# Performance work log

Measured on AMD Instinct MI355X. Metric: run time of the kernel, lower is better.

Reference implementation:

```python
import jax, jax.numpy as jnp
import numpy as np

N_NODES = 100_000
N_EDGES = 3_200_000
EPS_BN = 1e-5
EPS_NORM = 1e-12


def _sage_conv(x, src, dst, ew, pw, pb, lw, lb, rw, n_nodes):
    # project=True: relu(Linear_in->in) applied to source features
    xp = jax.nn.relu(x @ pw + pb)                       # [N, in]
    msg = xp[src] * ew[:, None]                         # [E, in] gather + weight
    agg = jax.ops.segment_sum(msg, dst, num_segments=n_nodes)      # scatter-sum
    cnt = jax.ops.segment_sum(jnp.ones_like(ew), dst, num_segments=n_nodes)
    mean = agg / jnp.maximum(cnt, 1.0)[:, None]         # scatter-mean
    out = mean @ lw + lb + x @ rw                       # neighbor lin + root lin
    # normalize=True: L2 normalize rows
    nrm = jnp.sqrt(jnp.sum(out * out, axis=-1, keepdims=True))
    return out / jnp.maximum(nrm, EPS_NORM)


def setup_inputs() -> dict:
    key = jax.random.key(0)
    ks = jax.random.split(key, 20)
    d = {}
    d["h"] = jax.random.normal(ks[0], (N_NODES, 5), dtype=jnp.float32)
    d["edge_index"] = jax.random.randint(ks[1], (2, N_EDGES), 0, N_NODES, dtype=jnp.int32)
    d["edge_weight"] = jax.random.uniform(ks[2], (N_EDGES,), dtype=jnp.float32)
    # BatchNorm1d(5) params (conv2_norm in the source is unused in forward)
    d["bn_gamma"] = jnp.ones((5,), jnp.float32)
    d["bn_beta"] = jnp.zeros((5,), jnp.float32)

    def lin(k, fan_in, fan_out):
        return jax.random.normal(k, (fan_in, fan_out), jnp.float32) * (1.0 / np.sqrt(fan_in))

    # conv1: 5 -> 64 ; conv2: 64 -> 64 (fixing source bug) ; conv3: 64 -> 5
    dims = [(5, 64), (64, 64), (64, 5)]
    ki = 3
    for i, (fi, fo) in enumerate(dims, start=1):
        d[f"c{i}_pw"] = lin(ks[ki], fi, fi); ki += 1
        d[f"c{i}_pb"] = jnp.zeros((fi,), jnp.float32)
        d[f"c{i}_lw"] = lin(ks[ki], fi, fo); ki += 1
        d[f"c{i}_lb"] = jnp.zeros((fo,), jnp.float32)
        d[f"c{i}_rw"] = lin(ks[ki], fi, fo); ki += 1
    return d


def reference(h, edge_index, edge_weight, bn_gamma, bn_beta,
              c1_pw, c1_pb, c1_lw, c1_lb, c1_rw,
              c2_pw, c2_pb, c2_lw, c2_lb, c2_rw,
              c3_pw, c3_pb, c3_lw, c3_lb, c3_rw):
    src, dst = edge_index[0], edge_index[1]
    # BatchNorm1d (training-mode batch statistics, biased variance)
    mu = jnp.mean(h, axis=0)
    var = jnp.mean((h - mu) ** 2, axis=0)
    x = (h - mu) * jax.lax.rsqrt(var + EPS_BN) * bn_gamma + bn_beta

    x = jax.nn.relu(_sage_conv(x, src, dst, edge_weight, c1_pw, c1_pb, c1_lw, c1_lb, c1_rw, N_NODES))
    x = jax.nn.relu(_sage_conv(x, src, dst, edge_weight, c2_pw, c2_pb, c2_lw, c2_lb, c2_rw, N_NODES))
    x = _sage_conv(x, src, dst, edge_weight, c3_pw, c3_pb, c3_lw, c3_lb, c3_rw, N_NODES)
    # dropout omitted (deterministic / eval-mode reference)
    return x
```

## Files before the change

### kernel.cpp

```cpp
#include <hip/hip_runtime.h>
#include <hip/hip_bf16.h>

#define N_NODES 100000
#define N_EDGES 3200000
#define BSH 8
#define NB 391

typedef __hip_bfloat16 bf16;

#define RL(v, k) __int_as_float(__builtin_amdgcn_readlane(__float_as_int(v), (k)))

__device__ __forceinline__ float loadF(const void* p, long long i, int isf32) {
    if (isf32) return ((const float*)p)[i];
    unsigned short v = ((const unsigned short*)p)[i];
    union { unsigned u; float f; } c;
    c.u = ((unsigned)v) << 16;
    return c.f;
}

__device__ __forceinline__ unsigned packEdge(int s, float w) {
    bf16 b = __float2bfloat16(w);
    unsigned short bits = *(unsigned short*)&b;
    return ((unsigned)s << 15) | (unsigned)(bits & 0x7FFF);
}
__device__ __forceinline__ int edgeSrc(unsigned u) { return (int)(u >> 15); }
__device__ __forceinline__ float edgeW(unsigned u) {
    union { unsigned x; float f; } c;
    c.x = (u & 0x7FFFu) << 16;
    return c.f;
}

#define W_GAMMA 0
#define W_BETA 8
#define W_C1PW 16
#define W_C1PB 48
#define W_C1LW 56
#define W_C1LB 376
#define W_C1RW 440
#define W_C2PW 760
#define W_C2PB 4856
#define W_C2LW 4920
#define W_C2LB 9016
#define W_C2RW 9080
#define W_C3PW 13176
#define W_C3PB 17272
#define W_C3LW 17336
#define W_C3LB 17656
#define W_C3RW 17664

__global__ void detect_dtype(const void* ew, int* flag) {
    const unsigned short* u = (const unsigned short*)ew;
    int lane = threadIdx.x;
    int big = 0;
    for (int i = lane; i < 1024; i += 64) {
        unsigned short v = u[2 * i];
        int ex = (v >> 7) & 0xFF;
        if (ex >= 128) big++;
    }
#pragma unroll
    for (int o = 32; o; o >>= 1) big += __shfl_xor(big, o, 64);
    if (lane == 0) *flag = (big > 100) ? 1 : 0;
}

__global__ void cvt_weights(const int* flag,
                            const void* p0, const void* p1, const void* p2, const void* p3,
                            const void* p4, const void* p5, const void* p6, const void* p7,
                            const void* p8, const void* p9, const void* p10, const void* p11,
                            const void* p12, const void* p13, const void* p14, const void* p15,
                            const void* p16, float* __restrict__ wts) {
    const void* ptrs[17] = {p0, p1, p2, p3, p4, p5, p6, p7, p8,
                            p9, p10, p11, p12, p13, p14, p15, p16};
    const int sz[17] = {5, 5, 25, 5, 320, 64, 320, 4096, 64,
                        4096, 64, 4096, 4096, 64, 320, 5, 320};
    const int off[17] = {W_GAMMA, W_BETA, W_C1PW, W_C1PB, W_C1LW, W_C1LB, W_C1RW,
                         W_C2PW, W_C2PB, W_C2LW, W_C2LB, W_C2RW,
                         W_C3PW, W_C3PB, W_C3LW, W_C3LB, W_C3RW};
    int t = blockIdx.x;
    int isf32 = *flag;
    for (int i = threadIdx.x; i < sz[t]; i += blockDim.x)
        wts[off[t] + i] = loadF(ptrs[t], i, isf32);
}

__global__ void bn_stats(const void* __restrict__ h, const int* __restrict__ flag,
                         float* __restrict__ stats) {
    int isf32 = *flag;
    float s[5] = {0, 0, 0, 0, 0}, q[5] = {0, 0, 0, 0, 0};
    int tid = blockIdx.x * blockDim.x + threadIdx.x;
    int stride = gridDim.x * blockDim.x;
    for (int i = tid; i < N_NODES; i += stride) {
#pragma unroll
        for (int f = 0; f < 5; f++) {
            float v = loadF(h, i * 5 + f, isf32);
            s[f] += v;
            q[f] += v * v;
        }
    }
#pragma unroll
    for (int f = 0; f < 5; f++) {
#pragma unroll
        for (int o = 32; o; o >>= 1) {
            s[f] += __shfl_xor(s[f], o, 64);
            q[f] += __shfl_xor(q[f], o, 64);
        }
    }
    __shared__ float ls[4][10];
    int wave = threadIdx.x >> 6, lane = threadIdx.x & 63;
    if (lane == 0) {
#pragma unroll
        for (int f = 0; f < 5; f++) { ls[wave][f] = s[f]; ls[wave][5 + f] = q[f]; }
    }
    __syncthreads();
    if (threadIdx.x < 10) {
        float v = ls[0][threadIdx.x] + ls[1][threadIdx.x] + ls[2][threadIdx.x] + ls[3][threadIdx.x];
        int idx = (threadIdx.x < 5) ? threadIdx.x : (threadIdx.x - 5 + 8);
        atomicAdd(&stats[idx], v);
    }
}

__global__ void bn_proj1(const void* __restrict__ h, const int* __restrict__ flag,
                         const float* __restrict__ stats, const float* __restrict__ wts,
                         float* __restrict__ xbn, float* __restrict__ xp1) {
    __shared__ float s_sc[5], s_sb[5];
    if (threadIdx.x < 5) {
        int f = threadIdx.x;
        float mean = stats[f] / (float)N_NODES;
        float var = stats[8 + f] / (float)N_NODES - mean * mean;
        float sc = wts[W_GAMMA + f] * rsqrtf(var + 1e-5f);
        s_sc[f] = sc;
        s_sb[f] = wts[W_BETA + f] - mean * sc;
    }
    __syncthreads();
    int isf32 = *flag;
    int i = blockIdx.x * blockDim.x + threadIdx.x;
    if (i >= N_NODES) return;
    float x[5];
#pragma unroll
    for (int f = 0; f < 5; f++)
        x[f] = loadF(h, i * 5 + f, isf32) * s_sc[f] + s_sb[f];
#pragma unroll
    for (int f = 0; f < 5; f++) xbn[i * 5 + f] = x[f];
#pragma unroll
    for (int j = 0; j < 5; j++) {
        float a = wts[W_C1PB + j];
#pragma unroll
        for (int k = 0; k < 5; k++) a += x[k] * wts[W_C1PW + k * 5 + j];
        xp1[i * 8 + j] = fmaxf(a, 0.f);
    }
}

__global__ void __launch_bounds__(256) bucket_hist(const int* __restrict__ dst,
                                                   int* __restrict__ bucketCnt) {
    __shared__ int hcnt[NB];
    for (int i = threadIdx.x; i < NB; i += 256) hcnt[i] = 0;
    __syncthreads();
    int per = (N_EDGES + gridDim.x - 1) / gridDim.x;
    int s = blockIdx.x * per;
    int e = min(s + per, N_EDGES);
    for (int i = s + threadIdx.x; i < e; i += 256)
        atomicAdd(&hcnt[dst[i] >> BSH], 1);
    __syncthreads();
    for (int i = threadIdx.x; i < NB; i += 256)
        if (hcnt[i]) atomicAdd(&bucketCnt[i], hcnt[i]);
}

__global__ void __launch_bounds__(512) bucket_scan(const int* __restrict__ bucketCnt,
                                                   int* __restrict__ bucketStart,
                                                   int* __restrict__ bucketCursor) {
    int tid = threadIdx.x, lane = tid & 63, w = tid >> 6;
    int v = (tid < NB) ? bucketCnt[tid] : 0;
    int sc = v;
#pragma unroll
    for (int o = 1; o < 64; o <<= 1) {
        int t = __shfl_up(sc, o, 64);
        if (lane >= o) sc += t;
    }
    __shared__ int ws[8];
    if (lane == 63) ws[w] = sc;
    __syncthreads();
    if (w == 0) {
        int wv = (lane < 8) ? ws[lane] : 0;
        int s2 = wv;
#pragma unroll
        for (int o = 1; o < 8; o <<= 1) {
            int t = __shfl_up(s2, o, 64);
            if (lane >= o) s2 += t;
        }
        if (lane < 8) ws[lane] = s2;
    }
    __syncthreads();
    int woff = w ? ws[w - 1] : 0;
    int ex = woff + sc - v;
    if (tid < NB) {
        bucketStart[tid] = ex;
        bucketCursor[tid] = ex;
    }
    if (tid == 0) bucketStart[NB] = N_EDGES;
}

__global__ void __launch_bounds__(256) bucket_stage(const int* __restrict__ src,
                                                    const int* __restrict__ dst,
                                                    const void* __restrict__ ew,
                                                    const int* __restrict__ flag,
                                                    int* __restrict__ bucketCursor,
                                                    uint2* __restrict__ stage) {
    __shared__ int hcnt[NB], cur[NB];
    int isf32 = *flag;
    for (int i = threadIdx.x; i < NB; i += 256) hcnt[i] = 0;
    __syncthreads();
    int per = (N_EDGES + gridDim.x - 1) / gridDim.x;
    int s = blockIdx.x * per;
    int e = min(s + per, N_EDGES);
    for (int i = s + threadIdx.x; i < e; i += 256)
        atomicAdd(&hcnt[dst[i] >> BSH], 1);
    __syncthreads();
    for (int i = threadIdx.x; i < NB; i += 256)
        cur[i] = hcnt[i] ? atomicAdd(&bucketCursor[i], hcnt[i]) : 0;
    __syncthreads();
    for (int i = s + threadIdx.x; i < e; i += 256) {
        int d = dst[i];
        int slot = atomicAdd(&cur[d >> BSH], 1);
        stage[slot] = make_uint2((unsigned)d, packEdge(src[i], loadF(ew, i, isf32)));
    }
}

__global__ void __launch_bounds__(256) bucket_place(const uint2* __restrict__ stage,
                                                    const int* __restrict__ bucketStart,
                                                    int* __restrict__ start,
                                                    unsigned* __restrict__ perm) {
    int b = blockIdx.x, tid = threadIdx.x;
    int base = bucketStart[b];
    int cnt = bucketStart[b + 1] - base;
    int n0 = b << BSH;
    int nn = min(256, N_NODES - n0);
    __shared__ int lcnt[256], loff[256], ws[4];
    lcnt[tid] = 0;
    __syncthreads();
    for (int i = tid; i < cnt; i += 256)
        atomicAdd(&lcnt[stage[base + i].x & 255], 1);
    __syncthreads();
    int lane = tid & 63, w = tid >> 6;
    int v = lcnt[tid];
    int sc = v;
#pragma unroll
    for (int o = 1; o < 64; o <<= 1) {
        int t = __shfl_up(sc, o, 64);
        if (lane >= o) sc += t;
    }
    if (lane == 63) ws[w] = sc;
    __syncthreads();
    int woff = 0;
    for (int k = 0; k < w; k++) woff += ws[k];
    loff[tid] = woff + sc - v;
    __syncthreads();
    if (tid < nn) start[n0 + tid] = base + loff[tid];
    if (b == 0 && tid == 0) start[N_NODES] = N_EDGES;
    lcnt[tid] = 0;
    __syncthreads();
    for (int i = tid; i < cnt; i += 256) {
        uint2 sv = stage[base + i];
        int l = sv.x & 255;
        int p = atomicAdd(&lcnt[l], 1);
        perm[base + loff[l] + p] = sv.y;
    }
}

__global__ void __launch_bounds__(256) conv1_fused(const float* __restrict__ xp1,
                                                   const float* __restrict__ xbn,
                                                   const int* __restrict__ start,
                                                   const unsigned* __restrict__ perm,
                                                   const float* __restrict__ wts,
                                                   float* __restrict__ x1,
                                                   bf16* __restrict__ y2) {
    int lane = threadIdx.x & 63;
    int wid = __builtin_amdgcn_readfirstlane((blockIdx.x * blockDim.x + threadIdx.x) >> 6);
    int nw = (gridDim.x * blockDim.x) >> 6;
    float Wlw[5], Wrw[5];
#pragma unroll
    for (int k = 0; k < 5; k++) {
        Wlw[k] = wts[W_C1LW + k * 64 + lane];
        Wrw[k] = wts[W_C1RW + k * 64 + lane];
    }
    float lb = wts[W_C1LB + lane];
    float W1[64], W2[64];
#pragma unroll
    for (int k = 0; k < 64; k++) W1[k] = wts[W_C2PW + k * 64 + lane];
#pragma unroll
    for (int k = 0; k < 64; k++) W2[k] = wts[W_C2LW + k * 64 + lane];
    float pb = wts[W_C2PB + lane];
    for (int node = wid; node < N_NODES; node += nw) {
        int e0 = start[node], e1 = start[node + 1];
        float s0 = 0, s1 = 0, s2 = 0, s3 = 0, s4 = 0;
        for (int eb = e0; eb < e1; eb += 64) {
            int e = eb + lane;
            if (e < e1) {
                unsigned p = perm[e];
                float w = edgeW(p);
                const float* row = xp1 + (size_t)edgeSrc(p) * 8;
                float4 v4 = *(const float4*)row;
                float v5 = row[4];
                s0 += v4.x * w; s1 += v4.y * w; s2 += v4.z * w;
                s3 += v4.w * w; s4 += v5 * w;
            }
        }
#pragma unroll
        for (int o = 32; o; o >>= 1) {
            s0 += __shfl_xor(s0, o, 64);
            s1 += __shfl_xor(s1, o, 64);
            s2 += __shfl_xor(s2, o, 64);
            s3 += __shfl_xor(s3, o, 64);
            s4 += __shfl_xor(s4, o, 64);
        }
        float ic = 1.f / fmaxf((float)(e1 - e0), 1.f);
        float xb = (lane < 5) ? xbn[node * 5 + lane] : 0.f;
        float out = lb + s0 * ic * Wlw[0] + s1 * ic * Wlw[1] + s2 * ic * Wlw[2] +
                    s3 * ic * Wlw[3] + s4 * ic * Wlw[4];
#pragma unroll
        for (int k = 0; k < 5; k++) out += RL(xb, k) * Wrw[k];
        float ss = out * out;
#pragma unroll
        for (int o = 32; o; o >>= 1) ss += __shfl_xor(ss, o, 64);
        float xv = fmaxf(out / fmaxf(sqrtf(ss), 1e-12f), 0.f);
        x1[(size_t)node * 64 + lane] = xv;
        float a0 = pb, a1 = 0.f, a2 = 0.f, a3 = 0.f;
#pragma unroll
        for (int k = 0; k < 64; k += 4) {
            a0 += RL(xv, k) * W1[k];
            a1 += RL(xv, k + 1) * W1[k + 1];
            a2 += RL(xv, k + 2) * W1[k + 2];
            a3 += RL(xv, k + 3) * W1[k + 3];
        }
        float xp = fmaxf((a0 + a1) + (a2 + a3), 0.f);
        float b0 = 0.f, b1 = 0.f, b2 = 0.f, b3 = 0.f;
#pragma unroll
        for (int k = 0; k < 64; k += 4) {
            b0 += RL(xp, k) * W2[k];
            b1 += RL(xp, k + 1) * W2[k + 1];
            b2 += RL(xp, k + 2) * W2[k + 2];
            b3 += RL(xp, k + 3) * W2[k + 3];
        }
        y2[(size_t)node * 64 + lane] = __float2bfloat16((b0 + b1) + (b2 + b3));
    }
}

__global__ void __launch_bounds__(256) conv2_fused_reg(const bf16* __restrict__ y2,
                                                       const int* __restrict__ start,
                                                       const unsigned* __restrict__ perm,
                                                       const float* __restrict__ x1,
                                                       const float* __restrict__ wts,
                                                       float* __restrict__ x2) {
    int lane = threadIdx.x & 63;
    int wid = __builtin_amdgcn_readfirstlane((blockIdx.x * blockDim.x + threadIdx.x) >> 6);
    int nw = (gridDim.x * blockDim.x) >> 6;
    float W[64];
#pragma unroll
    for (int k = 0; k < 64; k++) W[k] = wts[W_C2RW + k * 64 + lane];
    float lb = wts[W_C2LB + lane];
    for (int node = wid; node < N_NODES; node += nw) {
        int e0 = start[node], e1 = start[node + 1];
        float acc = 0.f;
        int e = e0;
        for (; e + 16 <= e1; e += 16) {
            unsigned p[16];
#pragma unroll
            for (int u = 0; u < 16; u++) p[u] = perm[e + u];
            float v[16];
#pragma unroll
            for (int u = 0; u < 16; u++)
                v[u] = __bfloat162float(y2[(size_t)edgeSrc(p[u]) * 64 + lane]);
#pragma unroll
            for (int u = 0; u < 16; u++) acc += v[u] * edgeW(p[u]);
        }
        for (; e + 4 <= e1; e += 4) {
            unsigned p[4];
#pragma unroll
            for (int u = 0; u < 4; u++) p[u] = perm[e + u];
            float v[4];
#pragma unroll
            for (int u = 0; u < 4; u++)
                v[u] = __bfloat162float(y2[(size_t)edgeSrc(p[u]) * 64 + lane]);
#pragma unroll
            for (int u = 0; u < 4; u++) acc += v[u] * edgeW(p[u]);
        }
        for (; e < e1; e++) {
            unsigned p = perm[e];
            acc += __bfloat162float(y2[(size_t)edgeSrc(p) * 64 + lane]) * edgeW(p);
        }
        float ic = 1.f / fmaxf((float)(e1 - e0), 1.f);
        float xv = x1[(size_t)node * 64 + lane];
        float o0 = acc * ic + lb, o1 = 0.f, o2 = 0.f, o3 = 0.f;
#pragma unroll
        for (int k = 0; k < 64; k += 4) {
            o0 += RL(xv, k) * W[k];
            o1 += RL(xv, k + 1) * W[k + 1];
            o2 += RL(xv, k + 2) * W[k + 2];
            o3 += RL(xv, k + 3) * W[k + 3];
        }
        float out = (o0 + o1) + (o2 + o3);
        float ss = out * out;
#pragma unroll
        for (int o = 32; o; o >>= 1) ss += __shfl_xor(ss, o, 64);
        float v = out / fmaxf(sqrtf(ss), 1e-12f);
        x2[(size_t)node * 64 + lane] = fmaxf(v, 0.f);
    }
}

__global__ void __launch_bounds__(256) proj3_reg(const float* __restrict__ x2,
                                                 const float* __restrict__ wts,
                                                 float* __restrict__ y3) {
    int lane = threadIdx.x & 63;
    int wid = __builtin_amdgcn_readfirstlane((blockIdx.x * blockDim.x + threadIdx.x) >> 6);
    int nw = (gridDim.x * blockDim.x) >> 6;
    float W1[64], Wl[5];
#pragma unroll
    for (int k = 0; k < 64; k++) W1[k] = wts[W_C3PW + k * 64 + lane];
#pragma unroll
    for (int j = 0; j < 5; j++) Wl[j] = wts[W_C3LW + lane * 5 + j];
    float pb = wts[W_C3PB + lane];
    for (int node = wid; node < N_NODES; node += nw) {
        float xv = x2[(size_t)node * 64 + lane];
        float a0 = pb, a1 = 0.f, a2 = 0.f, a3 = 0.f;
#pragma unroll
        for (int k = 0; k < 64; k += 4) {
            a0 += RL(xv, k) * W1[k];
            a1 += RL(xv, k + 1) * W1[k + 1];
            a2 += RL(xv, k + 2) * W1[k + 2];
            a3 += RL(xv, k + 3) * W1[k + 3];
        }
        float xp = fmaxf((a0 + a1) + (a2 + a3), 0.f);
#pragma unroll
        for (int j = 0; j < 5; j++) {
            float p = xp * Wl[j];
#pragma unroll
            for (int o = 32; o; o >>= 1) p += __shfl_xor(p, o, 64);
            if (lane == j) y3[(size_t)node * 8 + j] = p;
        }
    }
}

__global__ void __launch_bounds__(256) conv3_fused(const float* __restrict__ y3,
                                                   const float* __restrict__ x2,
                                                   const int* __restrict__ start,
                                                   const unsigned* __restrict__ perm,
                                                   const float* __restrict__ wts,
                                                   const int* __restrict__ flag,
                                                   void* __restrict__ outp) {
    int lane = threadIdx.x & 63;
    int wid = __builtin_amdgcn_readfirstlane((blockIdx.x * blockDim.x + threadIdx.x) >> 6);
    int nw = (gridDim.x * blockDim.x) >> 6;
    float Wr[5];
#pragma unroll
    for (int j = 0; j < 5; j++) Wr[j] = wts[W_C3RW + lane * 5 + j];
    float lb3[5];
#pragma unroll
    for (int j = 0; j < 5; j++) lb3[j] = wts[W_C3LB + j];
    int isf32 = *flag;
    for (int node = wid; node < N_NODES; node += nw) {
        int e0 = start[node], e1 = start[node + 1];
        float s0 = 0, s1 = 0, s2 = 0, s3 = 0, s4 = 0;
        for (int eb = e0; eb < e1; eb += 64) {
            int e = eb + lane;
            if (e < e1) {
                unsigned p = perm[e];
                float w = edgeW(p);
                const float* row = y3 + (size_t)edgeSrc(p) * 8;
                float4 v4 = *(const float4*)row;
                float v5 = row[4];
                s0 += v4.x * w; s1 += v4.y * w; s2 += v4.z * w;
                s3 += v4.w * w; s4 += v5 * w;
            }
        }
#pragma unroll
        for (int o = 32; o; o >>= 1) {
            s0 += __shfl_xor(s0, o, 64);
            s1 += __shfl_xor(s1, o, 64);
            s2 += __shfl_xor(s2, o, 64);
            s3 += __shfl_xor(s3, o, 64);
            s4 += __shfl_xor(s4, o, 64);
        }
        float ic = 1.f / fmaxf((float)(e1 - e0), 1.f);
        float xv = x2[(size_t)node * 64 + lane];
        float m[5] = {s0 * ic, s1 * ic, s2 * ic, s3 * ic, s4 * ic};
        float r[5], ss = 0.f;
#pragma unroll
        for (int j = 0; j < 5; j++) {
            float p = xv * Wr[j];
#pragma unroll
            for (int o = 32; o; o >>= 1) p += __shfl_xor(p, o, 64);
            r[j] = p + m[j] + lb3[j];
            ss += r[j] * r[j];
        }
        float inv = 1.f / fmaxf(sqrtf(ss), 1e-12f);
#pragma unroll
        for (int j = 0; j < 5; j++) {
            if (lane == j) {
                float v = r[j] * inv;
                if (isf32) ((float*)outp)[node * 5 + j] = v;
                else ((bf16*)outp)[node * 5 + j] = __float2bfloat16(v);
            }
        }
    }
}

extern "C" void kernel_launch(void* const* d_in, const int* in_sizes, int n_in,
                              void* d_out, int out_size, void* d_ws, size_t ws_size,
                              hipStream_t stream) {
    const void* h = d_in[0];
    const int* ei = (const int*)d_in[1];
    const int* src = ei;
    const int* dst = ei + N_EDGES;
    const void* ew = d_in[2];

    float* W = (float*)d_ws;
    int* flag = (int*)W;
    float* stats = W + 16;
    float* wts = W + 64;
    float* xbn = W + 20480;
    float* xp1 = xbn + N_NODES * 5;
    int* startp = (int*)(xp1 + N_NODES * 8);
    int* bucketCnt = startp + N_NODES + 64;
    int* bucketStart = bucketCnt + NB + 1;
    int* bucketCursor = bucketStart + NB + 1;
    unsigned* perm = (unsigned*)(bucketCursor + NB + 62);
    float* x1 = (float*)(perm + N_EDGES);
    uint2* stage = (uint2*)x1;
    bf16* y2 = (bf16*)(x1 + (size_t)N_NODES * 64);
    float* x2 = x1;
    float* y3 = xp1;

    detect_dtype<<<1, 64, 0, stream>>>(ew, flag);
    cvt_weights<<<17, 256, 0, stream>>>(flag,
        d_in[3], d_in[4],
        d_in[5], d_in[6], d_in[7], d_in[8], d_in[9],
        d_in[10], d_in[11], d_in[12], d_in[13], d_in[14],
        d_in[15], d_in[16], d_in[17], d_in[18], d_in[19],
        wts);

    hipMemsetAsync(stats, 0, 32 * sizeof(float), stream);
    hipMemsetAsync(bucketCnt, 0, NB * sizeof(int), stream);

    bn_stats<<<200, 256, 0, stream>>>(h, flag, stats);
    bn_proj1<<<(N_NODES + 255) / 256, 256, 0, stream>>>(h, flag, stats, wts, xbn, xp1);

    bucket_hist<<<512, 256, 0, stream>>>(dst, bucketCnt);
    bucket_scan<<<1, 512, 0, stream>>>(bucketCnt, bucketStart, bucketCursor);
    bucket_stage<<<512, 256, 0, stream>>>(src, dst, ew, flag, bucketCursor, stage);
    bucket_place<<<NB, 256, 0, stream>>>(stage, bucketStart, startp, perm);

    conv1_fused<<<2048, 256, 0, stream>>>(xp1, xbn, startp, perm, wts, x1, y2);

    conv2_fused_reg<<<4096, 256, 0, stream>>>(y2, startp, perm, x1, wts, x2);

    proj3_reg<<<2048, 256, 0, stream>>>(x2, wts, y3);
    conv3_fused<<<2048, 256, 0, stream>>>(y3, x2, startp, perm, wts, flag, d_out);
}
```

Before: 572.4 us.

## Make conv2 aggregation edge-parallel per 64-node block with LDS atomics

Replaces the wave-per-node conv2 kernel with a block-per-64-nodes kernel. Each wave takes contiguous 16-edge chunks of the block's CSR edge range and accumulates weighted neighbor features into a shared-memory tile using LDS atomic adds. A new pre-pass writes a per-edge byte giving each edge's local destination slot; it reuses the xp1 scratch buffer. The aim is better load balance across irregular node degrees and fewer short tail loops. The cost is an extra kernel launch, an extra byte read per edge, and LDS atomic traffic. The root linear layer is also batched over 16 nodes per wave, so each weight chunk is reused across those nodes.

New measurement: 1.670 ms. 2.92x slower.

```diff
diff --git a/kernel.cpp b/kernel.cpp
--- a/kernel.cpp
+++ b/kernel.cpp
@@ -342,65 +342,100 @@
     }
 }
 
-__global__ void __launch_bounds__(256) conv2_fused_reg(const bf16* __restrict__ y2,
-                                                       const int* __restrict__ start,
-                                                       const unsigned* __restrict__ perm,
-                                                       const float* __restrict__ x1,
-                                                       const float* __restrict__ wts,
-                                                       float* __restrict__ x2) {
+__global__ void __launch_bounds__(256) dstloc_fill(const int* __restrict__ start,
+                                                   unsigned char* __restrict__ dstloc) {
     int lane = threadIdx.x & 63;
-    int wid = __builtin_amdgcn_readfirstlane((blockIdx.x * blockDim.x + threadIdx.x) >> 6);
+    int wid = (blockIdx.x * blockDim.x + threadIdx.x) >> 6;
     int nw = (gridDim.x * blockDim.x) >> 6;
-    float W[64];
-#pragma unroll
-    for (int k = 0; k < 64; k++) W[k] = wts[W_C2RW + k * 64 + lane];
-    float lb = wts[W_C2LB + lane];
     for (int node = wid; node < N_NODES; node += nw) {
         int e0 = start[node], e1 = start[node + 1];
-        float acc = 0.f;
-        int e = e0;
-        for (; e + 16 <= e1; e += 16) {
+        unsigned char v = (unsigned char)(node & 63);
+        for (int e = e0 + lane; e < e1; e += 64) dstloc[e] = v;
+    }
+}
+
+__global__ void __launch_bounds__(256) conv2_lds(const bf16* __restrict__ y2,
+                                                 const int* __restrict__ start,
+                                                 const unsigned* __restrict__ perm,
+                                                 const unsigned char* __restrict__ dstloc,
+                                                 const float* __restrict__ x1,
+                                                 const float* __restrict__ wts,
+                                                 float* __restrict__ x2) {
+    __shared__ float s_acc[64 * 64];
+    int tid = threadIdx.x;
+    int lane = tid & 63;
+    int w = tid >> 6;
+    int gbase = blockIdx.x * 64;
+#pragma unroll
+    for (int i = 0; i < 16; i++) s_acc[tid + i * 256] = 0.f;
+    int gend = min(gbase + 64, N_NODES);
+    int e0 = start[gbase];
+    int e1 = start[gend];
+    __syncthreads();
+    for (int ce = e0 + w * 16; ce < e1; ce += 64) {
+        int m = e1 - ce;
+        if (m >= 16) {
             unsigned p[16];
 #pragma unroll
-            for (int u = 0; u < 16; u++) p[u] = perm[e + u];
+            for (int u = 0; u < 16; u++) p[u] = perm[ce + u];
+            int dl[16];
+#pragma unroll
+            for (int u = 0; u < 16; u++) dl[u] = dstloc[ce + u];
             float v[16];
 #pragma unroll
             for (int u = 0; u < 16; u++)
-                v[u] = __bfloat162float(y2[(size_t)edgeSrc(p[u]) * 64 + lane]);
-#pragma unroll
-            for (int u = 0; u < 16; u++) acc += v[u] * edgeW(p[u]);
-        }
-        for (; e + 4 <= e1; e += 4) {
-            unsigned p[4];
-#pragma unroll
-            for (int u = 0; u < 4; u++) p[u] = perm[e + u];
-            float v[4];
-#pragma unroll
-            for (int u = 0; u < 4; u++)
-                v[u] = __bfloat162float(y2[(size_t)edgeSrc(p[u]) * 64 + lane]);
-#pragma unroll
-            for (int u = 0; u < 4; u++) acc += v[u] * edgeW(p[u]);
-        }
-        for (; e < e1; e++) {
-            unsigned p = perm[e];
-            acc += __bfloat162float(y2[(size_t)edgeSrc(p) * 64 + lane]) * edgeW(p);
-        }
-        float ic = 1.f / fmaxf((float)(e1 - e0), 1.f);
-        float xv = x1[(size_t)node * 64 + lane];
-        float o0 = acc * ic + lb, o1 = 0.f, o2 = 0.f, o3 = 0.f;
-#pragma unroll
-        for (int k = 0; k < 64; k += 4) {
-            o0 += RL(xv, k) * W[k];
-            o1 += RL(xv, k + 1) * W[k + 1];
-            o2 += RL(xv, k + 2) * W[k + 2];
-            o3 += RL(xv, k + 3) * W[k + 3];
-        }
-        float out = (o0 + o1) + (o2 + o3);
+                v[u] = __bfloat162float(y2[(size_t)(p[u] >> 15) * 64 + lane]);
+#pragma unroll
+            for (int u = 0; u < 16; u++)
+                atomicAdd(&s_acc[dl[u] * 64 + lane], v[u] * edgeW(p[u]));
+        } else {
+            for (int u = 0; u < m; u++) {
+                unsigned pp = perm[ce + u];
+                int dl = dstloc[ce + u];
+                float vv = __bfloat162float(y2[(size_t)(pp >> 15) * 64 + lane]);
+                atomicAdd(&s_acc[dl * 64 + lane], vv * edgeW(pp));
+            }
+        }
+    }
+    __syncthreads();
+    int nb = w * 16;
+    float lb = wts[W_C2LB + lane];
+    float xv[16], outv[16];
+#pragma unroll
+    for (int n = 0; n < 16; n++) {
+        int node = gbase + nb + n;
+        if (node < N_NODES) {
+            float a = s_acc[(nb + n) * 64 + lane];
+            int d0 = start[node], d1 = start[node + 1];
+            xv[n] = x1[(size_t)node * 64 + lane];
+            outv[n] = a / fmaxf((float)(d1 - d0), 1.f) + lb;
+        } else {
+            xv[n] = 0.f;
+            outv[n] = 0.f;
+        }
+    }
+#pragma unroll
+    for (int c = 0; c < 4; c++) {
+        float Wc[16];
+#pragma unroll
+        for (int j = 0; j < 16; j++) Wc[j] = wts[W_C2RW + (c * 16 + j) * 64 + lane];
+#pragma unroll
+        for (int n = 0; n < 16; n++) {
+#pragma unroll
+            for (int j = 0; j < 16; j++)
+                outv[n] += RL(xv[n], c * 16 + j) * Wc[j];
+        }
+    }
+#pragma unroll
+    for (int n = 0; n < 16; n++) {
+        int node = gbase + nb + n;
+        if (node >= N_NODES) continue;
+        float out = outv[n];
         float ss = out * out;
 #pragma unroll
         for (int o = 32; o; o >>= 1) ss += __shfl_xor(ss, o, 64);
-        float v = out / fmaxf(sqrtf(ss), 1e-12f);
-        x2[(size_t)node * 64 + lane] = fmaxf(v, 0.f);
+        float vv = out / fmaxf(sqrtf(ss), 1e-12f);
+        x2[(size_t)node * 64 + lane] = fmaxf(vv, 0.f);
     }
 }
 
@@ -525,6 +560,7 @@
     uint2* stage = (uint2*)x1;
     bf16* y2 = (bf16*)(x1 + (size_t)N_NODES * 64);
     float* x2 = x1;
+    unsigned char* dstloc = (unsigned char*)xp1;
     float* y3 = xp1;
 
     detect_dtype<<<1, 64, 0, stream>>>(ew, flag);
@@ -548,7 +584,8 @@
 
     conv1_fused<<<2048, 256, 0, stream>>>(xp1, xbn, startp, perm, wts, x1, y2);
 
-    conv2_fused_reg<<<4096, 256, 0, stream>>>(y2, startp, perm, x1, wts, x2);
+    dstloc_fill<<<512, 256, 0, stream>>>(startp, dstloc);
+    conv2_lds<<<(N_NODES + 63) / 64, 256, 0, stream>>>(y2, startp, perm, dstloc, x1, wts, x2);
 
     proj3_reg<<<2048, 256, 0, stream>>>(x2, wts, y3);
     conv3_fused<<<2048, 256, 0, stream>>>(y3, x2, startp, perm, wts, flag, d_out);
```

## Split conv1 gather from conv2 projections and block projections over node tiles

Applied to the files above, without the earlier changes.

Conv1 is split into a gather-only kernel and a separate projection kernel. The gather now gives each edge 8 lanes, one per padded feature, and loads 4 edges per lane per iteration for more memory-level parallelism. The two 64x64 projections move to a kernel that handles 16 nodes per wave, so each weight chunk loaded into registers is reused across 16 nodes instead of holding 128 weight registers for every node. xp1 padding columns are zeroed so the 8-wide gather reads clean values. The cost is an extra kernel launch and a round trip of x1 through global memory.

Measured after the change: 558.9 us (median of 2 runs). -2.4%, faster.

```diff
diff --git a/kernel.cpp b/kernel.cpp
--- a/kernel.cpp
+++ b/kernel.cpp
@@ -146,6 +146,8 @@
         for (int k = 0; k < 5; k++) a += x[k] * wts[W_C1PW + k * 5 + j];
         xp1[i * 8 + j] = fmaxf(a, 0.f);
     }
+#pragma unroll
+    for (int j = 5; j < 8; j++) xp1[i * 8 + j] = 0.f;
 }
 
 __global__ void __launch_bounds__(256) bucket_hist(const int* __restrict__ dst,
@@ -264,14 +266,14 @@
     }
 }
 
-__global__ void __launch_bounds__(256) conv1_fused(const float* __restrict__ xp1,
-                                                   const float* __restrict__ xbn,
-                                                   const int* __restrict__ start,
-                                                   const unsigned* __restrict__ perm,
-                                                   const float* __restrict__ wts,
-                                                   float* __restrict__ x1,
-                                                   bf16* __restrict__ y2) {
+__global__ void __launch_bounds__(256) conv1_gather(const float* __restrict__ xp1,
+                                                    const float* __restrict__ xbn,
+                                                    const int* __restrict__ start,
+                                                    const unsigned* __restrict__ perm,
+                                                    const float* __restrict__ wts,
+                                                    float* __restrict__ x1) {
     int lane = threadIdx.x & 63;
+    int slot = lane >> 3, f = lane & 7;
     int wid = __builtin_amdgcn_readfirstlane((blockIdx.x * blockDim.x + threadIdx.x) >> 6);
     int nw = (gridDim.x * blockDim.x) >> 6;
     float Wlw[5], Wrw[5];
@@ -281,64 +283,91 @@
         Wrw[k] = wts[W_C1RW + k * 64 + lane];
     }
     float lb = wts[W_C1LB + lane];
-    float W1[64], W2[64];
-#pragma unroll
-    for (int k = 0; k < 64; k++) W1[k] = wts[W_C2PW + k * 64 + lane];
-#pragma unroll
-    for (int k = 0; k < 64; k++) W2[k] = wts[W_C2LW + k * 64 + lane];
-    float pb = wts[W_C2PB + lane];
     for (int node = wid; node < N_NODES; node += nw) {
         int e0 = start[node], e1 = start[node + 1];
-        float s0 = 0, s1 = 0, s2 = 0, s3 = 0, s4 = 0;
-        for (int eb = e0; eb < e1; eb += 64) {
-            int e = eb + lane;
-            if (e < e1) {
-                unsigned p = perm[e];
-                float w = edgeW(p);
-                const float* row = xp1 + (size_t)edgeSrc(p) * 8;
-                float4 v4 = *(const float4*)row;
-                float v5 = row[4];
-                s0 += v4.x * w; s1 += v4.y * w; s2 += v4.z * w;
-                s3 += v4.w * w; s4 += v5 * w;
+        float acc = 0.f;
+        for (int eb = e0; eb < e1; eb += 32) {
+            unsigned p[4];
+#pragma unroll
+            for (int q = 0; q < 4; q++) {
+                int e = eb + q * 8 + slot;
+                p[q] = (e < e1) ? perm[e] : 0u;
             }
-        }
-#pragma unroll
-        for (int o = 32; o; o >>= 1) {
-            s0 += __shfl_xor(s0, o, 64);
-            s1 += __shfl_xor(s1, o, 64);
-            s2 += __shfl_xor(s2, o, 64);
-            s3 += __shfl_xor(s3, o, 64);
-            s4 += __shfl_xor(s4, o, 64);
-        }
+            float v[4];
+#pragma unroll
+            for (int q = 0; q < 4; q++)
+                v[q] = xp1[(size_t)(p[q] >> 15) * 8 + f];
+#pragma unroll
+            for (int q = 0; q < 4; q++)
+                acc += v[q] * edgeW(p[q]);
+        }
+        acc += __shfl_xor(acc, 8, 64);
+        acc += __shfl_xor(acc, 16, 64);
+        acc += __shfl_xor(acc, 32, 64);
         float ic = 1.f / fmaxf((float)(e1 - e0), 1.f);
         float xb = (lane < 5) ? xbn[node * 5 + lane] : 0.f;
-        float out = lb + s0 * ic * Wlw[0] + s1 * ic * Wlw[1] + s2 * ic * Wlw[2] +
-                    s3 * ic * Wlw[3] + s4 * ic * Wlw[4];
-#pragma unroll
-        for (int k = 0; k < 5; k++) out += RL(xb, k) * Wrw[k];
+        float out = lb;
+#pragma unroll
+        for (int k = 0; k < 5; k++)
+            out += RL(acc, k) * ic * Wlw[k] + RL(xb, k) * Wrw[k];
         float ss = out * out;
 #pragma unroll
         for (int o = 32; o; o >>= 1) ss += __shfl_xor(ss, o, 64);
         float xv = fmaxf(out / fmaxf(sqrtf(ss), 1e-12f), 0.f);
         x1[(size_t)node * 64 + lane] = xv;
-        float a0 = pb, a1 = 0.f, a2 = 0.f, a3 = 0.f;
-#pragma unroll
-        for (int k = 0; k < 64; k += 4) {
-            a0 += RL(xv, k) * W1[k];
-            a1 += RL(xv, k + 1) * W1[k + 1];
-            a2 += RL(xv, k + 2) * W1[k + 2];
-            a3 += RL(xv, k + 3) * W1[k + 3];
-        }
-        float xp = fmaxf((a0 + a1) + (a2 + a3), 0.f);
-        float b0 = 0.f, b1 = 0.f, b2 = 0.f, b3 = 0.f;
-#pragma unroll
-        for (int k = 0; k < 64; k += 4) {
-            b0 += RL(xp, k) * W2[k];
-            b1 += RL(xp, k + 1) * W2[k + 1];
-            b2 += RL(xp, k + 2) * W2[k + 2];
-            b3 += RL(xp, k + 3) * W2[k + 3];
-        }
-        y2[(size_t)node * 64 + lane] = __float2bfloat16((b0 + b1) + (b2 + b3));
+    }
+}
+
+__global__ void __launch_bounds__(256) proj2_blocked(const float* __restrict__ x1,
+                                                     const float* __restrict__ wts,
+                                                     bf16* __restrict__ y2) {
+    int lane = threadIdx.x & 63;
+    int wid = (blockIdx.x * blockDim.x + threadIdx.x) >> 6;
+    int nb = wid * 16;
+    if (nb >= N_NODES) return;
+    float xv[16];
+#pragma unroll
+    for (int n = 0; n < 16; n++) {
+        int node = nb + n;
+        xv[n] = (node < N_NODES) ? x1[(size_t)node * 64 + lane] : 0.f;
+    }
+    float a[16];
+    float pb = wts[W_C2PB + lane];
+#pragma unroll
+    for (int n = 0; n < 16; n++) a[n] = pb;
+#pragma unroll
+    for (int c = 0; c < 4; c++) {
+        float Wc[16];
+#pragma unroll
+        for (int j = 0; j < 16; j++) Wc[j] = wts[W_C2PW + (c * 16 + j) * 64 + lane];
+#pragma unroll
+        for (int n = 0; n < 16; n++) {
+#pragma unroll
+            for (int j = 0; j < 16; j++)
+                a[n] += RL(xv[n], c * 16 + j) * Wc[j];
+        }
+    }
+#pragma unroll
+    for (int n = 0; n < 16; n++) a[n] = fmaxf(a[n], 0.f);
+    float b[16];
+#pragma unroll
+    for (int n = 0; n < 16; n++) b[n] = 0.f;
+#pragma unroll
+    for (int c = 0; c < 4; c++) {
+        float Wc[16];
+#pragma unroll
+        for (int j = 0; j < 16; j++) Wc[j] = wts[W_C2LW + (c * 16 + j) * 64 + lane];
+#pragma unroll
+        for (int n = 0; n < 16; n++) {
+#pragma unroll
+            for (int j = 0; j < 16; j++)
+                b[n] += RL(a[n], c * 16 + j) * Wc[j];
+        }
+    }
+#pragma unroll
+    for (int n = 0; n < 16; n++) {
+        int node = nb + n;
+        if (node < N_NODES) y2[(size_t)node * 64 + lane] = __float2bfloat16(b[n]);
     }
 }
 
@@ -546,7 +575,8 @@
     bucket_stage<<<512, 256, 0, stream>>>(src, dst, ew, flag, bucketCursor, stage);
     bucket_place<<<NB, 256, 0, stream>>>(stage, bucketStart, startp, perm);
 
-    conv1_fused<<<2048, 256, 0, stream>>>(xp1, xbn, startp, perm, wts, x1, y2);
+    conv1_gather<<<4096, 256, 0, stream>>>(xp1, xbn, startp, perm, wts, x1);
+    proj2_blocked<<<(N_NODES / 16 + 1 + 3) / 4, 256, 0, stream>>>(x1, wts, y2);
 
     conv2_fused_reg<<<4096, 256, 0, stream>>>(y2, startp, perm, x1, wts, x2);
 
```
